# Performance work log

Measured on AMD Instinct MI355X. Metric: run time of the kernel, lower is better.

Reference implementation:

```python
import jax, jax.numpy as jnp
import numpy as np

N_NODES = 100000
N_EDGES = 3200000
IN_DIM, HID_DIM, N_CLASS = 64, 32, 20


def setup_inputs() -> dict:
    key = jax.random.key(0)
    k1, k2, k3, k4, k5, k6 = jax.random.split(key, 6)
    x = jax.random.normal(k1, (N_NODES, IN_DIM), dtype=jnp.float32)
    edge_index = jax.random.randint(k2, (2, N_EDGES), 0, N_NODES, dtype=jnp.int64)
    W1 = jax.random.normal(k3, (IN_DIM, HID_DIM), dtype=jnp.float32) / np.sqrt(IN_DIM)
    b1 = jnp.zeros((HID_DIM,), dtype=jnp.float32)
    Wout = jax.random.normal(k4, (HID_DIM, N_CLASS), dtype=jnp.float32) / np.sqrt(HID_DIM)
    bout = jnp.zeros((N_CLASS,), dtype=jnp.float32)
    return {"x": x, "edge_index": edge_index, "W1": W1, "b1": b1, "Wout": Wout, "bout": bout}


def gcn_conv(x, edge_index, W, b):
    # PyG GCNConv defaults: add self-loops, symmetric deg^{-1/2} normalization.
    n = x.shape[0]
    loop = jnp.arange(n, dtype=edge_index.dtype)
    row = jnp.concatenate([edge_index[0], loop])  # source
    col = jnp.concatenate([edge_index[1], loop])  # target
    deg = jax.ops.segment_sum(jnp.ones_like(col, dtype=x.dtype), col, num_segments=n)
    dis = jnp.where(deg > 0, deg ** -0.5, 0.0)
    norm = dis[row] * dis[col]  # [E+N]
    xw = x @ W  # [N, HID]
    msg = norm[:, None] * xw[row]  # [E+N, HID]
    agg = jax.ops.segment_sum(msg, col, num_segments=n)
    return agg + b


def reference(x, edge_index, W1, b1, Wout, bout):
    h = gcn_conv(x, edge_index, W1, b1)
    emb = jax.nn.relu(h)
    return emb @ Wout + bout
```

## Files before the change

kernel.cpp:

```cpp
#include <hip/hip_runtime.h>
#include <hip/hip_fp16.h>
#include <math.h>

#define N_NODES 100000
#define N_EDGES 3200000
#define IN_DIM 64
#define HID_DIM 32
#define N_CLASS 20

#define BKT_BITS 6
#define BKT_W    64
#define NBKT     1563
#define CAP_BKT  2560
#define HALF_W   32
#define CAP_D    1536
#define ENT_R    (CAP_BKT / 256)

#define SUP_SHIFT 12
#define NS       25
#define CAP_S    132000
#define CH1      2048
#define NBLK1    ((N_EDGES + CH1 - 1) / CH1)
#define CH2      4096
#define BPS      ((CAP_S + CH2 - 1) / CH2)

__global__ void k_detect(const int* __restrict__ ei32, int* __restrict__ flag,
                         int* __restrict__ scursor, int* __restrict__ gcursor) {
    __shared__ int any;
    if (threadIdx.x == 0) any = 0;
    __syncthreads();
    int nz = 0;
    for (int k = threadIdx.x; k < 4096; k += blockDim.x)
        if (ei32[2 * k + 1] != 0) nz = 1;
    if (nz) atomicOr(&any, 1);
    for (int i = threadIdx.x; i < NBKT; i += blockDim.x) gcursor[i] = i * CAP_BKT;
    if (threadIdx.x < NS) scursor[threadIdx.x] = threadIdx.x * CAP_S;
    __syncthreads();
    if (threadIdx.x == 0) *flag = any ? 0 : 1;
}

__device__ __forceinline__ int get_idx(const int* __restrict__ ei32, int wide, int pos) {
    return wide ? ei32[2 * (long long)pos] : ei32[pos];
}

__global__ void __launch_bounds__(512, 4)
kS1(const int* __restrict__ ei32, const int* __restrict__ flag,
    int* __restrict__ scursor, unsigned int* __restrict__ sp) {
    __shared__ int lh[NS], lgb[NS], lrt[NS];
    int wide = *flag;
    if (threadIdx.x < NS) { lh[threadIdx.x] = 0; lrt[threadIdx.x] = 0; }
    __syncthreads();
    int base = blockIdx.x * CH1;
    int src[4], dst[4];
#pragma unroll
    for (int k = 0; k < 4; ++k) {
        int e = base + k * 512 + (int)threadIdx.x;
        if (e < N_EDGES) {
            src[k] = get_idx(ei32, wide, e);
            dst[k] = get_idx(ei32, wide, N_EDGES + e);
            atomicAdd(&lh[dst[k] >> SUP_SHIFT], 1);
        } else dst[k] = -1;
    }
    __syncthreads();
    if (threadIdx.x < NS && lh[threadIdx.x])
        lgb[threadIdx.x] = atomicAdd(&scursor[threadIdx.x], lh[threadIdx.x]);
    __syncthreads();
#pragma unroll
    for (int k = 0; k < 4; ++k) {
        if (dst[k] >= 0) {
            int s = dst[k] >> SUP_SHIFT;
            int r = atomicAdd(&lrt[s], 1);
            int pos = lgb[s] + r;
            if (pos < (s + 1) * CAP_S)
                sp[pos] = ((unsigned)src[k] << SUP_SHIFT) |
                          (unsigned)(dst[k] & ((1 << SUP_SHIFT) - 1));
        }
    }
}

__global__ void __launch_bounds__(512, 4)
kS2(const unsigned int* __restrict__ sp, const int* __restrict__ scursor,
    int* __restrict__ gcursor, unsigned int* __restrict__ pk) {
    __shared__ int lh[BKT_W], lgb[BKT_W], lrt[BKT_W];
    int s = blockIdx.x / BPS;
    int j = blockIdx.x % BPS;
    int sbase = s * CAP_S;
    int scount = min(scursor[s] - sbase, CAP_S);
    int start = j * CH2;
    if (start >= scount) return;
    int end = min(start + CH2, scount);
    if (threadIdx.x < BKT_W) { lh[threadIdx.x] = 0; lrt[threadIdx.x] = 0; }
    __syncthreads();
    unsigned ent[8]; int fb[8];
#pragma unroll
    for (int k = 0; k < 8; ++k) {
        int i = start + k * 512 + (int)threadIdx.x;
        if (i < end) {
            ent[k] = sp[sbase + i];
            fb[k] = (int)((ent[k] & ((1u << SUP_SHIFT) - 1)) >> BKT_BITS);
            atomicAdd(&lh[fb[k]], 1);
        } else fb[k] = -1;
    }
    __syncthreads();
    if (threadIdx.x < BKT_W && lh[threadIdx.x]) {
        int b = s * BKT_W + (int)threadIdx.x;
        if (b < NBKT) lgb[threadIdx.x] = atomicAdd(&gcursor[b], lh[threadIdx.x]);
    }
    __syncthreads();
#pragma unroll
    for (int k = 0; k < 8; ++k) {
        if (fb[k] >= 0) {
            int b = s * BKT_W + fb[k];
            int r = atomicAdd(&lrt[fb[k]], 1);
            int pos = lgb[fb[k]] + r;
            if (pos < (b + 1) * CAP_BKT)
                pk[pos] = ((ent[k] >> SUP_SHIFT) << BKT_BITS) | (ent[k] & (BKT_W - 1));
        }
    }
}

__global__ void kC1_deg(const unsigned int* __restrict__ pk, const int* __restrict__ gcursor,
                        float* __restrict__ dis) {
    __shared__ int lcnt[BKT_W];
    int b = blockIdx.x;
    int gb = b * CAP_BKT;
    int bsz = min(gcursor[b] - gb, CAP_BKT);
    if (threadIdx.x < BKT_W) lcnt[threadIdx.x] = 0;
    __syncthreads();
    for (int i = threadIdx.x; i < bsz; i += blockDim.x)
        atomicAdd(&lcnt[pk[gb + i] & (BKT_W - 1)], 1);
    __syncthreads();
    int node = b * BKT_W + threadIdx.x;
    if (threadIdx.x < BKT_W && node < N_NODES)
        dis[node] = rsqrtf((float)(lcnt[threadIdx.x] + 1));
}

__global__ void k_xw(const float* __restrict__ x, const float* __restrict__ W1,
                     const float* __restrict__ dis, __half* __restrict__ xw16) {
    __shared__ float sW[IN_DIM * HID_DIM];
    for (int i = threadIdx.x; i < IN_DIM * HID_DIM; i += blockDim.x) sW[i] = W1[i];
    __syncthreads();
    int tid = blockIdx.x * blockDim.x + threadIdx.x;
    int node = tid >> 3;
    int q = tid & 7;
    if (node >= N_NODES) return;
    const float4* xr = reinterpret_cast<const float4*>(x + (size_t)node * IN_DIM);
    float4 a = make_float4(0.f, 0.f, 0.f, 0.f);
#pragma unroll
    for (int k4 = 0; k4 < IN_DIM / 4; ++k4) {
        float4 xv = xr[k4];
        const float4 w0 = *reinterpret_cast<const float4*>(&sW[(k4 * 4 + 0) * HID_DIM + q * 4]);
        const float4 w1 = *reinterpret_cast<const float4*>(&sW[(k4 * 4 + 1) * HID_DIM + q * 4]);
        const float4 w2 = *reinterpret_cast<const float4*>(&sW[(k4 * 4 + 2) * HID_DIM + q * 4]);
        const float4 w3 = *reinterpret_cast<const float4*>(&sW[(k4 * 4 + 3) * HID_DIM + q * 4]);
        a.x += xv.x * w0.x + xv.y * w1.x + xv.z * w2.x + xv.w * w3.x;
        a.y += xv.x * w0.y + xv.y * w1.y + xv.z * w2.y + xv.w * w3.y;
        a.z += xv.x * w0.z + xv.y * w1.z + xv.z * w2.z + xv.w * w3.z;
        a.w += xv.x * w0.w + xv.y * w1.w + xv.z * w2.w + xv.w * w3.w;
    }
    float d = dis[node];
    union { __half2 h2[2]; uint2 u; } cvt;
    cvt.h2[0] = __floats2half2_rn(a.x * d, a.y * d);
    cvt.h2[1] = __floats2half2_rn(a.z * d, a.w * d);
    *reinterpret_cast<uint2*>(xw16 + (size_t)node * HID_DIM + q * 4) = cvt.u;
}

__device__ __forceinline__ void acc_row(float4& acc, uint2 u) {
    union U { unsigned u; __half2 hh; };
    U a0; a0.u = u.x; U a1; a1.u = u.y;
    float2 f0 = __half22float2(a0.hh);
    float2 f1 = __half22float2(a1.hh);
    acc.x += f0.x; acc.y += f0.y; acc.z += f1.x; acc.w += f1.y;
}

__global__ void __launch_bounds__(256, 8)
kD_gather(const unsigned int* __restrict__ pk, const int* __restrict__ gcursor,
          const float* __restrict__ dis, const __half* __restrict__ xw16,
          const float* __restrict__ b1, const float* __restrict__ Wout,
          const float* __restrict__ bout, float* __restrict__ out) {
    __shared__ int   ssrc[CAP_D];
    __shared__ int   lcnt[HALF_W], lstart[HALF_W], lrt[HALF_W];
    __shared__ int   stot;
    __shared__ float sW[HID_DIM * N_CLASS];
    __shared__ float sb1[HID_DIM];
    __shared__ float sbo[N_CLASS];
    for (int i = threadIdx.x; i < HID_DIM * N_CLASS; i += blockDim.x) sW[i] = Wout[i];
    if (threadIdx.x < HID_DIM) sb1[threadIdx.x] = b1[threadIdx.x];
    if (threadIdx.x < N_CLASS) sbo[threadIdx.x] = bout[threadIdx.x];
    if (threadIdx.x < HALF_W) { lcnt[threadIdx.x] = 0; lrt[threadIdx.x] = 0; }
    int B = blockIdx.x;
    int b = B >> 1, h = B & 1;
    int gb = b * CAP_BKT;
    int bsz = min(gcursor[b] - gb, CAP_BKT);
    __syncthreads();

    unsigned ents[ENT_R];
#pragma unroll
    for (int i = 0; i < ENT_R; ++i) {
        int idx = i * 256 + (int)threadIdx.x;
        ents[i] = (idx < bsz) ? pk[gb + idx] : 0xFFFFFFFFu;
    }
#pragma unroll
    for (int i = 0; i < ENT_R; ++i) {
        if (ents[i] != 0xFFFFFFFFu) {
            int ld = (int)(ents[i] & (BKT_W - 1));
            if ((ld >> 5) == h) atomicAdd(&lcnt[ld & (HALF_W - 1)], 1);
        }
    }
    __syncthreads();
    if (threadIdx.x < HALF_W) {
        int v = lcnt[threadIdx.x];
        int s = v;
#pragma unroll
        for (int d = 1; d < HALF_W; d <<= 1) {
            int t = __shfl_up(s, d, HALF_W);
            if ((int)(threadIdx.x & (HALF_W - 1)) >= d) s += t;
        }
        lstart[threadIdx.x] = s - v;
        if (threadIdx.x == HALF_W - 1) stot = s;
    }
    __syncthreads();
    bool fits = (stot <= CAP_D);
    if (fits) {
#pragma unroll
        for (int i = 0; i < ENT_R; ++i) {
            if (ents[i] != 0xFFFFFFFFu) {
                int ld = (int)(ents[i] & (BKT_W - 1));
                if ((ld >> 5) == h) {
                    int r = atomicAdd(&lrt[ld & (HALF_W - 1)], 1);
                    ssrc[lstart[ld & (HALF_W - 1)] + r] = (int)(ents[i] >> BKT_BITS);
                }
            }
        }
    }
    __syncthreads();

    int grp = threadIdx.x >> 3, part = threadIdx.x & 7;
    int ln = grp;
    int node = b * BKT_W + h * HALF_W + ln;
    if (node >= N_NODES) return;

    float4 acc = make_float4(0.f, 0.f, 0.f, 0.f);
    acc_row(acc, *reinterpret_cast<const uint2*>(xw16 + (size_t)node * HID_DIM + part * 4));
    float dc = dis[node];

    if (fits) {
        int s0 = lstart[ln], cnt = lcnt[ln];
        int e = s0, end = s0 + cnt;
        while (e + 8 <= end) {
            int srcs[8];
#pragma unroll
            for (int j = 0; j < 8; ++j) srcs[j] = ssrc[e + j];
            uint2 us[8];
#pragma unroll
            for (int j = 0; j < 8; ++j)
                us[j] = *reinterpret_cast<const uint2*>(xw16 + (size_t)srcs[j] * HID_DIM + part * 4);
#pragma unroll
            for (int j = 0; j < 8; ++j) acc_row(acc, us[j]);
            e += 8;
        }
        for (; e < end; ++e) {
            int src = ssrc[e];
            acc_row(acc, *reinterpret_cast<const uint2*>(xw16 + (size_t)src * HID_DIM + part * 4));
        }
    } else {
        int want = h * HALF_W + ln;
        for (int i = 0; i < bsz; ++i) {
            unsigned v = pk[gb + i];
            if ((int)(v & (BKT_W - 1)) == want)
                acc_row(acc, *reinterpret_cast<const uint2*>(xw16 + (size_t)(v >> BKT_BITS) * HID_DIM + part * 4));
        }
    }
    float e0 = fmaxf(dc * acc.x + sb1[part * 4 + 0], 0.f);
    float e1 = fmaxf(dc * acc.y + sb1[part * 4 + 1], 0.f);
    float e2 = fmaxf(dc * acc.z + sb1[part * 4 + 2], 0.f);
    float e3 = fmaxf(dc * acc.w + sb1[part * 4 + 3], 0.f);
    float o[N_CLASS];
#pragma unroll
    for (int cl = 0; cl < N_CLASS; ++cl) {
        o[cl] = e0 * sW[(part * 4 + 0) * N_CLASS + cl]
              + e1 * sW[(part * 4 + 1) * N_CLASS + cl]
              + e2 * sW[(part * 4 + 2) * N_CLASS + cl]
              + e3 * sW[(part * 4 + 3) * N_CLASS + cl];
    }
#pragma unroll
    for (int m = 1; m < 8; m <<= 1) {
#pragma unroll
        for (int cl = 0; cl < N_CLASS; ++cl) o[cl] += __shfl_xor(o[cl], m, 64);
    }
    if (part < 5) {
        float4 w = make_float4(o[part * 4 + 0] + sbo[part * 4 + 0],
                               o[part * 4 + 1] + sbo[part * 4 + 1],
                               o[part * 4 + 2] + sbo[part * 4 + 2],
                               o[part * 4 + 3] + sbo[part * 4 + 3]);
        *reinterpret_cast<float4*>(out + (size_t)node * N_CLASS + part * 4) = w;
    }
}

extern "C" void kernel_launch(void* const* d_in, const int* in_sizes, int n_in,
                              void* d_out, int out_size, void* d_ws, size_t ws_size,
                              hipStream_t stream) {
    const float* x    = (const float*)d_in[0];
    const int*   ei32 = (const int*)d_in[1];
    const float* W1   = (const float*)d_in[2];
    const float* b1   = (const float*)d_in[3];
    const float* Wout = (const float*)d_in[4];
    const float* bout = (const float*)d_in[5];
    float* out = (float*)d_out;

    unsigned int* sp      = (unsigned int*)d_ws;
    __half*       xw16    = (__half*)d_ws;
    unsigned int* pk      = sp + (size_t)NS * CAP_S;
    int*          gcursor = (int*)(pk + (size_t)NBKT * CAP_BKT);
    int*          scursor = gcursor + NBKT;
    float*        dis     = (float*)(scursor + NS);
    int*          flag    = (int*)(dis + N_NODES);

    k_detect<<<1, 256, 0, stream>>>(ei32, flag, scursor, gcursor);
    kS1<<<NBLK1, 512, 0, stream>>>(ei32, flag, scursor, sp);
    kS2<<<NS * BPS, 512, 0, stream>>>(sp, scursor, gcursor, pk);
    kC1_deg<<<NBKT, 256, 0, stream>>>(pk, gcursor, dis);
    k_xw<<<(N_NODES * 8 + 255) / 256, 256, 0, stream>>>(x, W1, dis, xw16);
    kD_gather<<<2 * NBKT, 256, 0, stream>>>(pk, gcursor, dis, xw16, b1, Wout, bout, out);
}
```

Before: 123.8 us.

## Process whole 64-node bucket per 512-thread block in gather kernel

```diff
diff --git a/kernel.cpp b/kernel.cpp
--- a/kernel.cpp
+++ b/kernel.cpp
@@ -12,9 +12,7 @@
 #define BKT_W    64
 #define NBKT     1563
 #define CAP_BKT  2560
-#define HALF_W   32
-#define CAP_D    1536
-#define ENT_R    (CAP_BKT / 256)
+#define ENT_R    (CAP_BKT / 512)
 
 #define SUP_SHIFT 12
 #define NS       25
@@ -173,23 +171,21 @@
     acc.x += f0.x; acc.y += f0.y; acc.z += f1.x; acc.w += f1.y;
 }
 
-__global__ void __launch_bounds__(256, 8)
+__global__ void __launch_bounds__(512, 8)
 kD_gather(const unsigned int* __restrict__ pk, const int* __restrict__ gcursor,
           const float* __restrict__ dis, const __half* __restrict__ xw16,
           const float* __restrict__ b1, const float* __restrict__ Wout,
           const float* __restrict__ bout, float* __restrict__ out) {
-    __shared__ int   ssrc[CAP_D];
-    __shared__ int   lcnt[HALF_W], lstart[HALF_W], lrt[HALF_W];
-    __shared__ int   stot;
+    __shared__ int   ssrc[CAP_BKT];
+    __shared__ int   lcnt[BKT_W], lstart[BKT_W], lrt[BKT_W];
     __shared__ float sW[HID_DIM * N_CLASS];
     __shared__ float sb1[HID_DIM];
     __shared__ float sbo[N_CLASS];
     for (int i = threadIdx.x; i < HID_DIM * N_CLASS; i += blockDim.x) sW[i] = Wout[i];
     if (threadIdx.x < HID_DIM) sb1[threadIdx.x] = b1[threadIdx.x];
     if (threadIdx.x < N_CLASS) sbo[threadIdx.x] = bout[threadIdx.x];
-    if (threadIdx.x < HALF_W) { lcnt[threadIdx.x] = 0; lrt[threadIdx.x] = 0; }
-    int B = blockIdx.x;
-    int b = B >> 1, h = B & 1;
+    if (threadIdx.x < BKT_W) { lcnt[threadIdx.x] = 0; lrt[threadIdx.x] = 0; }
+    int b = blockIdx.x;
     int gb = b * CAP_BKT;
     int bsz = min(gcursor[b] - gb, CAP_BKT);
     __syncthreads();
@@ -197,78 +193,69 @@
     unsigned ents[ENT_R];
 #pragma unroll
     for (int i = 0; i < ENT_R; ++i) {
-        int idx = i * 256 + (int)threadIdx.x;
+        int idx = i * 512 + (int)threadIdx.x;
         ents[i] = (idx < bsz) ? pk[gb + idx] : 0xFFFFFFFFu;
     }
+#pragma unroll
+    for (int i = 0; i < ENT_R; ++i)
+        if (ents[i] != 0xFFFFFFFFu) atomicAdd(&lcnt[ents[i] & (BKT_W - 1)], 1);
+    __syncthreads();
+    if (threadIdx.x < BKT_W) {
+        int v = lcnt[threadIdx.x];
+        int s = v;
+#pragma unroll
+        for (int d = 1; d < BKT_W; d <<= 1) {
+            int t = __shfl_up(s, d, BKT_W);
+            if ((int)threadIdx.x >= d) s += t;
+        }
+        lstart[threadIdx.x] = s - v;
+    }
+    __syncthreads();
 #pragma unroll
     for (int i = 0; i < ENT_R; ++i) {
         if (ents[i] != 0xFFFFFFFFu) {
             int ld = (int)(ents[i] & (BKT_W - 1));
-            if ((ld >> 5) == h) atomicAdd(&lcnt[ld & (HALF_W - 1)], 1);
-        }
-    }
-    __syncthreads();
-    if (threadIdx.x < HALF_W) {
-        int v = lcnt[threadIdx.x];
-        int s = v;
-#pragma unroll
-        for (int d = 1; d < HALF_W; d <<= 1) {
-            int t = __shfl_up(s, d, HALF_W);
-            if ((int)(threadIdx.x & (HALF_W - 1)) >= d) s += t;
-        }
-        lstart[threadIdx.x] = s - v;
-        if (threadIdx.x == HALF_W - 1) stot = s;
-    }
-    __syncthreads();
-    bool fits = (stot <= CAP_D);
-    if (fits) {
-#pragma unroll
-        for (int i = 0; i < ENT_R; ++i) {
-            if (ents[i] != 0xFFFFFFFFu) {
-                int ld = (int)(ents[i] & (BKT_W - 1));
-                if ((ld >> 5) == h) {
-                    int r = atomicAdd(&lrt[ld & (HALF_W - 1)], 1);
-                    ssrc[lstart[ld & (HALF_W - 1)] + r] = (int)(ents[i] >> BKT_BITS);
-                }
-            }
+            int r = atomicAdd(&lrt[ld], 1);
+            ssrc[lstart[ld] + r] = (int)(ents[i] >> BKT_BITS);
         }
     }
     __syncthreads();
 
     int grp = threadIdx.x >> 3, part = threadIdx.x & 7;
-    int ln = grp;
-    int node = b * BKT_W + h * HALF_W + ln;
+    int node = b * BKT_W + grp;
     if (node >= N_NODES) return;
 
     float4 acc = make_float4(0.f, 0.f, 0.f, 0.f);
     acc_row(acc, *reinterpret_cast<const uint2*>(xw16 + (size_t)node * HID_DIM + part * 4));
     float dc = dis[node];
 
-    if (fits) {
-        int s0 = lstart[ln], cnt = lcnt[ln];
-        int e = s0, end = s0 + cnt;
-        while (e + 8 <= end) {
-            int srcs[8];
-#pragma unroll
-            for (int j = 0; j < 8; ++j) srcs[j] = ssrc[e + j];
-            uint2 us[8];
-#pragma unroll
-            for (int j = 0; j < 8; ++j)
-                us[j] = *reinterpret_cast<const uint2*>(xw16 + (size_t)srcs[j] * HID_DIM + part * 4);
-#pragma unroll
-            for (int j = 0; j < 8; ++j) acc_row(acc, us[j]);
-            e += 8;
+    {
+        int e = lstart[grp], end = lstart[grp] + lcnt[grp];
+        while (e + 16 <= end) {
+            uint2 us[16];
+#pragma unroll
+            for (int j = 0; j < 16; ++j) {
+                int src = ssrc[e + j];
+                us[j] = *reinterpret_cast<const uint2*>(xw16 + (size_t)src * HID_DIM + part * 4);
+            }
+#pragma unroll
+            for (int j = 0; j < 16; ++j) acc_row(acc, us[j]);
+            e += 16;
+        }
+        while (e + 4 <= end) {
+            uint2 us[4];
+#pragma unroll
+            for (int j = 0; j < 4; ++j) {
+                int src = ssrc[e + j];
+                us[j] = *reinterpret_cast<const uint2*>(xw16 + (size_t)src * HID_DIM + part * 4);
+            }
+#pragma unroll
+            for (int j = 0; j < 4; ++j) acc_row(acc, us[j]);
+            e += 4;
         }
         for (; e < end; ++e) {
             int src = ssrc[e];
             acc_row(acc, *reinterpret_cast<const uint2*>(xw16 + (size_t)src * HID_DIM + part * 4));
-        }
-    } else {
-        int want = h * HALF_W + ln;
-        for (int i = 0; i < bsz; ++i) {
-            unsigned v = pk[gb + i];
-            if ((int)(v & (BKT_W - 1)) == want)
-                acc_row(acc, *reinterpret_cast<const uint2*>(xw16 + (size_t)(v >> BKT_BITS) * HID_DIM + part * 4));
         }
     }
     float e0 = fmaxf(dc * acc.x + sb1[part * 4 + 0], 0.f);
@@ -321,5 +308,5 @@
     kS2<<<NS * BPS, 512, 0, stream>>>(sp, scursor, gcursor, pk);
     kC1_deg<<<NBKT, 256, 0, stream>>>(pk, gcursor, dis);
     k_xw<<<(N_NODES * 8 + 255) / 256, 256, 0, stream>>>(x, W1, dis, xw16);
-    kD_gather<<<2 * NBKT, 256, 0, stream>>>(pk, gcursor, dis, xw16, b1, Wout, bout, out);
-}
+    kD_gather<<<NBKT, 512, 0, stream>>>(pk, gcursor, dis, xw16, b1, Wout, bout, out);
+}
```

Measured after the change: 123.0 us. No clear change (-0.6%).
